# Optimization experiments

Hardware: AMD Instinct MI355X
Metric: run time of the kernel (lower is better)

The kernel has to match this reference:

```python
import jax, jax.numpy as jnp
import numpy as np

B, S, DIM, H = 8, 1024, 1024, 16
HID = 512  # FeedForward default hidden_dim=512 (module passes only dim)
DH = DIM // H
EPS = 1e-5


def setup_inputs() -> dict:
    key = jax.random.key(0)
    ks = jax.random.split(key, 12)
    s = 1.0 / np.sqrt(DIM)
    return {
        "x": jax.random.normal(ks[0], (B, S, DIM), dtype=jnp.float32),
        "Wq": jax.random.normal(ks[1], (DIM, DIM), dtype=jnp.float32) * s,
        "Wk": jax.random.normal(ks[2], (DIM, DIM), dtype=jnp.float32) * s,
        "Wv": jax.random.normal(ks[3], (DIM, DIM), dtype=jnp.float32) * s,
        "Wo": jax.random.normal(ks[4], (DIM, DIM), dtype=jnp.float32) * s,
        "ln1_g": jnp.ones((DIM,), jnp.float32),
        "ln1_b": jnp.zeros((DIM,), jnp.float32),
        "W1": jax.random.normal(ks[5], (DIM, HID), dtype=jnp.float32) * s,
        "b1": jnp.zeros((HID,), jnp.float32),
        "W2": jax.random.normal(ks[6], (HID, DIM), dtype=jnp.float32) * (1.0 / np.sqrt(HID)),
        "b2": jnp.zeros((DIM,), jnp.float32),
        "ln2_g": jnp.ones((DIM,), jnp.float32),
        "ln2_b": jnp.zeros((DIM,), jnp.float32),
    }


def _layer_norm(x, g, b):
    mu = jnp.mean(x, axis=-1, keepdims=True)
    var = jnp.mean(jnp.square(x - mu), axis=-1, keepdims=True)
    return (x - mu) * jax.lax.rsqrt(var + EPS) * g + b


def reference(x, Wq, Wk, Wv, Wo, ln1_g, ln1_b, W1, b1, W2, b2, ln2_g, ln2_b):
    # Multi-head self-attention (dropout = identity at eval)
    def heads(t):  # [B,S,DIM] -> [B,H,S,DH]
        return t.reshape(B, S, H, DH).transpose(0, 2, 1, 3)

    q = heads(x @ Wq)
    k = heads(x @ Wk)
    v = heads(x @ Wv)
    scores = jnp.einsum("bhqd,bhkd->bhqk", q, k) / jnp.sqrt(jnp.float32(DH))
    attn = jax.nn.softmax(scores, axis=-1)
    ctx = jnp.einsum("bhqk,bhkd->bhqd", attn, v)
    ctx = ctx.transpose(0, 2, 1, 3).reshape(B, S, DIM)
    mha = ctx @ Wo

    h = _layer_norm(mha + x, ln1_g, ln1_b)
    ff = jax.nn.relu(h @ W1 + b1) @ W2 + b2
    out = _layer_norm(ff + h, ln2_g, ln2_b)
    return out
```

## Files before the change

### kernel.cpp

```cpp
#include <hip/hip_runtime.h>
#include <cstdint>
#include <cstddef>

#define DEV __device__ __forceinline__

typedef __bf16 bf16x8 __attribute__((ext_vector_type(8)));
typedef __bf16 bf16x4 __attribute__((ext_vector_type(4)));
typedef short  short4v __attribute__((ext_vector_type(4)));
typedef float  f32x4  __attribute__((ext_vector_type(4)));

static constexpr int Bb  = 8;
static constexpr int S   = 1024;
static constexpr int DIM = 1024;
static constexpr int H   = 16;
static constexpr int DH  = 64;
static constexpr int HID = 512;
static constexpr int M   = Bb * S;

DEV uint16_t f2bf(float f) {
  union { float f; uint32_t u; } v; v.f = f;
  uint32_t r = v.u + 0x7fffu + ((v.u >> 16) & 1u);
  return (uint16_t)(r >> 16);
}
DEV float bf2f(uint32_t u) {
  union { uint32_t u; float f; } v; v.u = u << 16;
  return v.f;
}

DEV void gl_lds16(const uint16_t* g, uint16_t* lds) {
  __builtin_amdgcn_global_load_lds(
      (const __attribute__((address_space(1))) void*)g,
      (__attribute__((address_space(3))) void*)lds, 16, 0, 0);
}

DEV bf16x8 ld8(const uint16_t* p) { return *reinterpret_cast<const bf16x8*>(p); }

#if __has_builtin(__builtin_amdgcn_mfma_f32_16x16x16bf16_1k)
DEV f32x4 mfma16(bf16x4 a, bf16x4 b, f32x4 c) {
  return __builtin_amdgcn_mfma_f32_16x16x16bf16_1k(
      __builtin_bit_cast(short4v, a), __builtin_bit_cast(short4v, b), c, 0, 0, 0);
}
#else
DEV f32x4 mfma16(bf16x4 a, bf16x4 b, f32x4 c) {
  asm volatile("v_mfma_f32_16x16x16_bf16 %0, %1, %2, %0" : "+v"(c) : "v"(a), "v"(b));
  return c;
}
#endif

DEV int swz(int row, int col) {
  return row * 64 + (((col >> 3) ^ (row & 7)) << 3) + (col & 7);
}

__global__ __launch_bounds__(256) void prep_all(const float* __restrict__ x,
                                                uint16_t* __restrict__ x16,
                                                const float* __restrict__ Wq,
                                                const float* __restrict__ Wk,
                                                const float* __restrict__ Wv,
                                                const float* __restrict__ Wo,
                                                const float* __restrict__ W1,
                                                const float* __restrict__ W2,
                                                uint16_t* __restrict__ wqkv_t,
                                                uint16_t* __restrict__ wo_t,
                                                uint16_t* __restrict__ w1_t,
                                                uint16_t* __restrict__ w2_t) {
  int bid = blockIdx.x;
  int tid = threadIdx.x;
  if (bid < 4096) {
    int i = (bid * 256 + tid) * 8;
    const float4* p = reinterpret_cast<const float4*>(x + i);
    float4 a = p[0], b = p[1];
    uint4 pk;
    pk.x = (uint32_t)f2bf(a.x) | ((uint32_t)f2bf(a.y) << 16);
    pk.y = (uint32_t)f2bf(a.z) | ((uint32_t)f2bf(a.w) << 16);
    pk.z = (uint32_t)f2bf(b.x) | ((uint32_t)f2bf(b.y) << 16);
    pk.w = (uint32_t)f2bf(b.z) | ((uint32_t)f2bf(b.w) << 16);
    *reinterpret_cast<uint4*>(x16 + i) = pk;
    return;
  }
  bid -= 4096;
  const float* src;
  uint16_t* dst;
  int R, C, bx, by;
  if (bid < 4096) {
    int which = bid >> 10, id = bid & 1023;
    if (which == 0)      { src = Wq; dst = wqkv_t; }
    else if (which == 1) { src = Wk; dst = wqkv_t + 1048576; }
    else if (which == 2) { src = Wv; dst = wqkv_t + 2097152; }
    else                 { src = Wo; dst = wo_t; }
    R = 1024; C = 1024; bx = id & 31; by = id >> 5;
  } else if (bid < 4608) {
    int id = bid - 4096;
    src = W1; dst = w1_t; R = 1024; C = 512; bx = id & 15; by = id >> 4;
  } else {
    int id = bid - 4608;
    src = W2; dst = w2_t; R = 512; C = 1024; bx = id & 31; by = id >> 5;
  }
  __shared__ float tile[32][33];
  int c0 = bx * 32, r0 = by * 32;
  int tx = tid & 31, ty = tid >> 5;
  #pragma unroll
  for (int i = 0; i < 4; i++)
    tile[ty + i * 8][tx] = src[(size_t)(r0 + ty + i * 8) * C + c0 + tx];
  __syncthreads();
  #pragma unroll
  for (int i = 0; i < 4; i++)
    dst[(size_t)(c0 + ty + i * 8) * R + r0 + tx] = f2bf(tile[tx][ty + i * 8]);
}

template <int BIAS, int RELU, int FUSEV>
__global__ __launch_bounds__(256) void gemm128p(const uint16_t* __restrict__ A,
                                                const uint16_t* __restrict__ Bt,
                                                const float* __restrict__ bias,
                                                uint16_t* __restrict__ Cout,
                                                uint16_t* __restrict__ vt,
                                                int N, int K) {
  __shared__ __align__(16) uint16_t As[2][128 * 64];
  __shared__ __align__(16) uint16_t Bs[2][128 * 64];
  const int tid = threadIdx.x;
  const int w = tid >> 6, l = tid & 63;
  const int hi = l >> 4, c = l & 15;
  int nwg = gridDim.x * gridDim.y;
  int lin = blockIdx.y * gridDim.x + blockIdx.x;
  if (!(nwg & 7)) lin = (lin & 7) * (nwg >> 3) + (lin >> 3);
  const int bx = lin % gridDim.x, by = lin / gridDim.x;
  const int m0 = by * 128, n0 = bx * 128;
  const int wr = (w >> 1) * 64, wc = (w & 1) * 64;
  const uint16_t* Ag = A + (size_t)m0 * K;
  const uint16_t* Bg = Bt + (size_t)n0 * K;
  f32x4 acc[4][4] = {};

  const int srow = tid >> 3;
  const int scol = ((tid & 7) ^ (srow & 7)) * 8;
  auto stage = [&](int k0, int buf) {
    #pragma unroll
    for (int i = 0; i < 4; i++)
      gl_lds16(Ag + (size_t)(i * 32 + srow) * K + k0 + scol,
               &As[buf][(i * 256 + w * 64) * 8]);
    #pragma unroll
    for (int i = 0; i < 4; i++)
      gl_lds16(Bg + (size_t)(i * 32 + srow) * K + k0 + scol,
               &Bs[buf][(i * 256 + w * 64) * 8]);
  };

  stage(0, 0);
  stage(64, 1);
  asm volatile("s_waitcnt vmcnt(8)" ::: "memory");
  __builtin_amdgcn_s_barrier();

  const int NTK = K >> 6;
  for (int t = 0; t < NTK; t++) {
    const int cur = t & 1;
    const uint16_t* Ab = As[cur];
    const uint16_t* Bb = Bs[cur];
    bf16x8 af[4][2], bfr[4][2];
    #pragma unroll
    for (int i = 0; i < 4; i++)
      #pragma unroll
      for (int kk = 0; kk < 2; kk++) {
        af[i][kk]  = ld8(&Ab[swz(wr + i * 16 + c, kk * 32 + hi * 8)]);
        bfr[i][kk] = ld8(&Bb[swz(wc + i * 16 + c, kk * 32 + hi * 8)]);
      }
    #pragma unroll
    for (int i = 0; i < 4; i++)
      #pragma unroll
      for (int j = 0; j < 4; j++) {
        acc[i][j] = __builtin_amdgcn_mfma_f32_16x16x32_bf16(af[i][0], bfr[j][0], acc[i][j], 0, 0, 0);
        acc[i][j] = __builtin_amdgcn_mfma_f32_16x16x32_bf16(af[i][1], bfr[j][1], acc[i][j], 0, 0, 0);
      }
    if (t == NTK - 1) break;
    asm volatile("s_waitcnt lgkmcnt(0)" ::: "memory");
    __builtin_amdgcn_s_barrier();
    if (t + 2 < NTK) {
      stage((t + 2) << 6, cur);
      asm volatile("s_waitcnt vmcnt(8)" ::: "memory");
    } else {
      asm volatile("s_waitcnt vmcnt(0)" ::: "memory");
    }
    __builtin_amdgcn_s_barrier();
  }

  const int r0 = m0 + wr + hi * 4;
  const int c0 = n0 + wc + c;
  if (FUSEV && c0 >= 2048) {
    #pragma unroll
    for (int j = 0; j < 4; j++) {
      int hd = c0 + j * 16 - 2048;
      #pragma unroll
      for (int i = 0; i < 4; i++) {
        int row = r0 + i * 16;
        size_t vi = ((size_t)(row >> 10) * 1024 + hd) * 1024 + (row & 1023);
        uint2 pk;
        pk.x = (uint32_t)f2bf(acc[i][j][0]) | ((uint32_t)f2bf(acc[i][j][1]) << 16);
        pk.y = (uint32_t)f2bf(acc[i][j][2]) | ((uint32_t)f2bf(acc[i][j][3]) << 16);
        *(uint2*)&vt[vi] = pk;
      }
    }
  } else {
    #pragma unroll
    for (int j = 0; j < 4; j++) {
      int col = c0 + j * 16;
      float bv = BIAS ? bias[col] : 0.0f;
      #pragma unroll
      for (int i = 0; i < 4; i++) {
        #pragma unroll
        for (int r = 0; r < 4; r++) {
          float v = acc[i][j][r] + bv;
          if (RELU) v = fmaxf(v, 0.0f);
          Cout[(size_t)(r0 + i * 16 + r) * N + col] = f2bf(v);
        }
      }
    }
  }
}

__global__ __launch_bounds__(256, 4) void attn12(const uint16_t* __restrict__ qkv,
                                                 const uint16_t* __restrict__ vt,
                                                 uint16_t* __restrict__ ctx) {
  int blk = blockIdx.x;
  int xcd = blk & 7, idx = blk >> 3;
  int qt = idx & 7;
  int bh = xcd + 8 * (idx >> 3);
  int h = bh & 15, b = bh >> 4;
  int q0 = qt * 128;
  int tid = threadIdx.x;
  int w = tid >> 6, l = tid & 63;
  int hi = l >> 4, c = l & 15;

  __shared__ __align__(16) uint16_t Klds[2][64 * 64];
  __shared__ __align__(16) uint16_t Vlds[2][64 * 64];

  constexpr float C2 = 0.125f * 1.44269504f;
  const uint16_t* qbase = qkv + (size_t)(b * S + q0 + w * 32) * 3072 + h * 64;
  bf16x8 aq[2][2];
  #pragma unroll
  for (int qg = 0; qg < 2; qg++)
    #pragma unroll
    for (int dk = 0; dk < 2; dk++) {
      bf16x8 v = ld8(qbase + (size_t)(qg * 16 + c) * 3072 + dk * 32 + hi * 8);
      #pragma unroll
      for (int e = 0; e < 8; e++) v[e] = (__bf16)((float)v[e] * C2);
      aq[qg][dk] = v;
    }

  f32x4 acc[2][4] = {};
  float psum[2] = {};

  const uint16_t* kgbase = qkv + (size_t)(b * S) * 3072 + 1024 + h * 64;
  const uint16_t* vgbase = vt + (size_t)(b * 16 + h) * 64 * S;

  const int lr = l >> 3, lc = l & 7;
  const int scol = (lc ^ lr) * 8;
  auto stage = [&](int kt, int buf) {
    #pragma unroll
    for (int i = 0; i < 2; i++) {
      int slab = w * 2 + i;
      gl_lds16(kgbase + (size_t)(kt + slab * 8 + lr) * 3072 + scol,
               &Klds[buf][slab * 512]);
      gl_lds16(vgbase + (size_t)(slab * 8 + lr) * S + kt + scol,
               &Vlds[buf][slab * 512]);
    }
  };

  stage(0, 0);
  asm volatile("s_waitcnt vmcnt(0)" ::: "memory");
  __syncthreads();

  constexpr int NT = S / 64;
  for (int t = 0; t < NT; t++) {
    int cur = t & 1;
    if (t + 1 < NT) stage((t + 1) * 64, cur ^ 1);

    #pragma unroll
    for (int kb = 0; kb < 4; kb++) {
      bf16x8 kf0 = ld8(&Klds[cur][swz(kb * 16 + c, hi * 8)]);
      bf16x8 kf1 = ld8(&Klds[cur][swz(kb * 16 + c, 32 + hi * 8)]);
      bf16x4 pb[2];
      __builtin_amdgcn_s_setprio(1);
      f32x4 z0 = {0.f, 0.f, 0.f, 0.f}, z1 = {0.f, 0.f, 0.f, 0.f};
      z0 = __builtin_amdgcn_mfma_f32_16x16x32_bf16(kf0, aq[0][0], z0, 0, 0, 0);
      z0 = __builtin_amdgcn_mfma_f32_16x16x32_bf16(kf1, aq[0][1], z0, 0, 0, 0);
      z1 = __builtin_amdgcn_mfma_f32_16x16x32_bf16(kf0, aq[1][0], z1, 0, 0, 0);
      z1 = __builtin_amdgcn_mfma_f32_16x16x32_bf16(kf1, aq[1][1], z1, 0, 0, 0);
      __builtin_amdgcn_s_setprio(0);
      #pragma unroll
      for (int r = 0; r < 4; r++) {
        float p0 = exp2f(z0[r]);
        float p1 = exp2f(z1[r]);
        psum[0] += p0;
        psum[1] += p1;
        pb[0][r] = (__bf16)p0;
        pb[1][r] = (__bf16)p1;
      }
      __builtin_amdgcn_s_setprio(1);
      #pragma unroll
      for (int db = 0; db < 4; db++) {
        bf16x4 va = *(const bf16x4*)&Vlds[cur][swz(db * 16 + c, kb * 16 + hi * 4)];
        acc[0][db] = mfma16(va, pb[0], acc[0][db]);
        acc[1][db] = mfma16(va, pb[1], acc[1][db]);
      }
      __builtin_amdgcn_s_setprio(0);
    }

    if (t + 1 < NT) {
      asm volatile("s_waitcnt vmcnt(0)" ::: "memory");
      __syncthreads();
    }
  }

  #pragma unroll
  for (int qg = 0; qg < 2; qg++) {
    psum[qg] += __shfl_xor(psum[qg], 16);
    psum[qg] += __shfl_xor(psum[qg], 32);
  }

  __syncthreads();

  uint16_t* Bw = &Vlds[w >> 1][(w & 1) * 2048];
  #pragma unroll
  for (int qg = 0; qg < 2; qg++) {
    float inv = 1.0f / psum[qg];
    int q = qg * 16 + c;
    #pragma unroll
    for (int db = 0; db < 4; db++) {
      uint2 pk;
      pk.x = (uint32_t)f2bf(acc[qg][db][0] * inv) |
             ((uint32_t)f2bf(acc[qg][db][1] * inv) << 16);
      pk.y = (uint32_t)f2bf(acc[qg][db][2] * inv) |
             ((uint32_t)f2bf(acc[qg][db][3] * inv) << 16);
      int chunk4 = (db * 4 + hi) ^ (q & 15);
      *(uint2*)&Bw[q * 64 + chunk4 * 4] = pk;
    }
  }
  int rrow = l >> 3, rch = l & 7;
  size_t gq0 = (size_t)(b * S + q0 + w * 32);
  #pragma unroll
  for (int it = 0; it < 4; it++) {
    int row = it * 8 + rrow;
    int k0 = (2 * rch) ^ (row & 15);
    int base = (k0 & ~1) * 4;
    uint4 v = *(const uint4*)&Bw[row * 64 + base];
    if (row & 1) { uint32_t t0 = v.x, t1 = v.y; v.x = v.z; v.y = v.w; v.z = t0; v.w = t1; }
    *(uint4*)&ctx[(gq0 + row) * DIM + h * 64 + rch * 8] = v;
  }
}

__global__ __launch_bounds__(256) void ln1_w(const uint16_t* __restrict__ a16,
                                             const uint16_t* __restrict__ x16,
                                             const float* __restrict__ g,
                                             const float* __restrict__ beta,
                                             uint16_t* __restrict__ h16) {
  int w = threadIdx.x >> 6, l = threadIdx.x & 63;
  size_t row = (size_t)blockIdx.x * 4 + w;
  const uint16_t* ap = a16 + row * DIM + l * 16;
  const uint16_t* xp = x16 + row * DIM + l * 16;
  uint4 av0 = *(const uint4*)ap, av1 = *(const uint4*)(ap + 8);
  uint4 xv0 = *(const uint4*)xp, xv1 = *(const uint4*)(xp + 8);
  float v[16];
  const uint32_t* au0 = (const uint32_t*)&av0;
  const uint32_t* au1 = (const uint32_t*)&av1;
  const uint32_t* xu0 = (const uint32_t*)&xv0;
  const uint32_t* xu1 = (const uint32_t*)&xv1;
  #pragma unroll
  for (int j = 0; j < 4; j++) {
    v[j * 2]     = bf2f(au0[j] & 0xffff) + bf2f(xu0[j] & 0xffff);
    v[j * 2 + 1] = bf2f(au0[j] >> 16)    + bf2f(xu0[j] >> 16);
    v[8 + j * 2]     = bf2f(au1[j] & 0xffff) + bf2f(xu1[j] & 0xffff);
    v[8 + j * 2 + 1] = bf2f(au1[j] >> 16)    + bf2f(xu1[j] >> 16);
  }
  float s = 0.f, sq = 0.f;
  #pragma unroll
  for (int j = 0; j < 16; j++) { s += v[j]; sq += v[j] * v[j]; }
  #pragma unroll
  for (int off = 32; off >= 1; off >>= 1) {
    s += __shfl_xor(s, off);
    sq += __shfl_xor(sq, off);
  }
  float mu = s * (1.0f / DIM);
  float var = sq * (1.0f / DIM) - mu * mu;
  float rstd = rsqrtf(var + 1e-5f);
  const float4* gp = (const float4*)(g + l * 16);
  const float4* bp = (const float4*)(beta + l * 16);
  uint4 o0, o1;
  uint32_t* ou0 = (uint32_t*)&o0;
  uint32_t* ou1 = (uint32_t*)&o1;
  #pragma unroll
  for (int q = 0; q < 2; q++) {
    float4 gv = gp[q], bv = bp[q];
    float e0 = (v[q * 4 + 0] - mu) * rstd * gv.x + bv.x;
    float e1 = (v[q * 4 + 1] - mu) * rstd * gv.y + bv.y;
    float e2 = (v[q * 4 + 2] - mu) * rstd * gv.z + bv.z;
    float e3 = (v[q * 4 + 3] - mu) * rstd * gv.w + bv.w;
    ou0[q * 2]     = (uint32_t)f2bf(e0) | ((uint32_t)f2bf(e1) << 16);
    ou0[q * 2 + 1] = (uint32_t)f2bf(e2) | ((uint32_t)f2bf(e3) << 16);
    float4 gv2 = gp[2 + q], bv2 = bp[2 + q];
    float f0 = (v[8 + q * 4 + 0] - mu) * rstd * gv2.x + bv2.x;
    float f1 = (v[8 + q * 4 + 1] - mu) * rstd * gv2.y + bv2.y;
    float f2 = (v[8 + q * 4 + 2] - mu) * rstd * gv2.z + bv2.z;
    float f3 = (v[8 + q * 4 + 3] - mu) * rstd * gv2.w + bv2.w;
    ou1[q * 2]     = (uint32_t)f2bf(f0) | ((uint32_t)f2bf(f1) << 16);
    ou1[q * 2 + 1] = (uint32_t)f2bf(f2) | ((uint32_t)f2bf(f3) << 16);
  }
  uint16_t* hp = h16 + row * DIM + l * 16;
  *(uint4*)hp = o0;
  *(uint4*)(hp + 8) = o1;
}

__global__ __launch_bounds__(256) void ln2_w(const uint16_t* __restrict__ ff16,
                                             const uint16_t* __restrict__ h16,
                                             const float* __restrict__ g,
                                             const float* __restrict__ beta,
                                             float* __restrict__ out_f) {
  int w = threadIdx.x >> 6, l = threadIdx.x & 63;
  size_t row = (size_t)blockIdx.x * 4 + w;
  const uint16_t* ap = ff16 + row * DIM + l * 16;
  const uint16_t* xp = h16 + row * DIM + l * 16;
  uint4 av0 = *(const uint4*)ap, av1 = *(const uint4*)(ap + 8);
  uint4 xv0 = *(const uint4*)xp, xv1 = *(const uint4*)(xp + 8);
  float v[16];
  const uint32_t* au0 = (const uint32_t*)&av0;
  const uint32_t* au1 = (const uint32_t*)&av1;
  const uint32_t* xu0 = (const uint32_t*)&xv0;
  const uint32_t* xu1 = (const uint32_t*)&xv1;
  #pragma unroll
  for (int j = 0; j < 4; j++) {
    v[j * 2]     = bf2f(au0[j] & 0xffff) + bf2f(xu0[j] & 0xffff);
    v[j * 2 + 1] = bf2f(au0[j] >> 16)    + bf2f(xu0[j] >> 16);
    v[8 + j * 2]     = bf2f(au1[j] & 0xffff) + bf2f(xu1[j] & 0xffff);
    v[8 + j * 2 + 1] = bf2f(au1[j] >> 16)    + bf2f(xu1[j] >> 16);
  }
  float s = 0.f, sq = 0.f;
  #pragma unroll
  for (int j = 0; j < 16; j++) { s += v[j]; sq += v[j] * v[j]; }
  #pragma unroll
  for (int off = 32; off >= 1; off >>= 1) {
    s += __shfl_xor(s, off);
    sq += __shfl_xor(sq, off);
  }
  float mu = s * (1.0f / DIM);
  float var = sq * (1.0f / DIM) - mu * mu;
  float rstd = rsqrtf(var + 1e-5f);
  const float4* gp = (const float4*)(g + l * 16);
  const float4* bp = (const float4*)(beta + l * 16);
  float* op = out_f + row * DIM + l * 16;
  #pragma unroll
  for (int q = 0; q < 4; q++) {
    float4 gv = gp[q], bv = bp[q];
    float4 o;
    o.x = (v[q * 4 + 0] - mu) * rstd * gv.x + bv.x;
    o.y = (v[q * 4 + 1] - mu) * rstd * gv.y + bv.y;
    o.z = (v[q * 4 + 2] - mu) * rstd * gv.z + bv.z;
    o.w = (v[q * 4 + 3] - mu) * rstd * gv.w + bv.w;
    *(float4*)(op + q * 4) = o;
  }
}

extern "C" void kernel_launch(void* const* d_in, const int* in_sizes, int n_in,
                              void* d_out, int out_size, void* d_ws, size_t ws_size,
                              hipStream_t stream) {
  const float* x    = (const float*)d_in[0];
  const float* Wq   = (const float*)d_in[1];
  const float* Wk   = (const float*)d_in[2];
  const float* Wv   = (const float*)d_in[3];
  const float* Wo   = (const float*)d_in[4];
  const float* ln1g = (const float*)d_in[5];
  const float* ln1b = (const float*)d_in[6];
  const float* W1   = (const float*)d_in[7];
  const float* b1   = (const float*)d_in[8];
  const float* W2   = (const float*)d_in[9];
  const float* b2   = (const float*)d_in[10];
  const float* ln2g = (const float*)d_in[11];
  const float* ln2b = (const float*)d_in[12];
  float* out = (float*)d_out;

  char* ws = (char*)d_ws;
  uint16_t* wqkv_t = (uint16_t*)(ws + 0);
  uint16_t* wo_t   = (uint16_t*)(ws + 6291456);
  uint16_t* w1_t   = (uint16_t*)(ws + 8388608);
  uint16_t* w2_t   = (uint16_t*)(ws + 9437184);
  uint16_t* x16    = (uint16_t*)(ws + 10485760);
  uint16_t* qkv16  = (uint16_t*)(ws + 27262976);
  uint16_t* mha16  = (uint16_t*)(ws + 27262976);
  uint16_t* ff16   = (uint16_t*)(ws + 27262976);
  uint16_t* h16    = (uint16_t*)(ws + 60817408);
  uint16_t* vt16   = (uint16_t*)(ws + 77594624);
  uint16_t* mid16  = vt16;
  uint16_t* ctx16  = (uint16_t*)(ws + 94371840);

  prep_all<<<9216, 256, 0, stream>>>(x, x16, Wq, Wk, Wv, Wo, W1, W2,
                                     wqkv_t, wo_t, w1_t, w2_t);
  gemm128p<0, 0, 1><<<dim3(24, 64), 256, 0, stream>>>(x16, wqkv_t, nullptr,
                                                      qkv16, vt16, 3072, DIM);
  attn12<<<1024, 256, 0, stream>>>(qkv16, vt16, ctx16);
  gemm128p<0, 0, 0><<<dim3(8, 64), 256, 0, stream>>>(ctx16, wo_t, nullptr,
                                                     mha16, nullptr, DIM, DIM);
  ln1_w<<<2048, 256, 0, stream>>>(mha16, x16, ln1g, ln1b, h16);
  gemm128p<1, 1, 0><<<dim3(4, 64), 256, 0, stream>>>(h16, w1_t, b1,
                                                     mid16, nullptr, HID, DIM);
  gemm128p<1, 0, 0><<<dim3(8, 64), 256, 0, stream>>>(mid16, w2_t, b2,
                                                     ff16, nullptr, DIM, HID);
  ln2_w<<<2048, 256, 0, stream>>>(ff16, h16, ln2g, ln2b, out);
}
```

Before: 221.5 us.

## Use 256x256-tile 8-wave GEMM with interleaved staging for QKV projection

Adds a new GEMM kernel for the fused QKV projection. It uses 512 threads and 256x256 output tiles, with each wave computing 128x64. Global-to-LDS staging of the next A/B halves is interleaved between four MFMA phases, and s_setprio raises priority around the MFMA sections. The larger tile raises arithmetic intensity and cuts redundant global loads, at the cost of more LDS (128KB), more registers and fewer workgroups (384). The fused V-transpose epilogue moves into the new kernel and is dropped from the older template.

```diff
diff --git a/kernel.cpp b/kernel.cpp
--- a/kernel.cpp
+++ b/kernel.cpp
@@ -107,12 +107,175 @@
     dst[(size_t)(c0 + ty + i * 8) * R + r0 + tx] = f2bf(tile[tx][ty + i * 8]);
 }
 
-template <int BIAS, int RELU, int FUSEV>
+__global__ __launch_bounds__(512, 2) void gemm8p(const uint16_t* __restrict__ A,
+                                                 const uint16_t* __restrict__ Bt,
+                                                 uint16_t* __restrict__ Cout,
+                                                 uint16_t* __restrict__ vt,
+                                                 int N, int K) {
+  __shared__ __align__(16) uint16_t As[2][2][128 * 64];
+  __shared__ __align__(16) uint16_t Bs[2][2][128 * 64];
+  const int tid = threadIdx.x;
+  const int w = tid >> 6, l = tid & 63;
+  const int hi = l >> 4, c = l & 15;
+  const int wr = w >> 2, wc = w & 3;
+  int nwg = gridDim.x * gridDim.y;
+  int lin = blockIdx.y * gridDim.x + blockIdx.x;
+  if (!(nwg & 7)) lin = (lin & 7) * (nwg >> 3) + (lin >> 3);
+  const int bx = lin % gridDim.x, by = lin / gridDim.x;
+  const int m0 = by * 256, n0 = bx * 256;
+  const uint16_t* Ag = A + (size_t)m0 * K;
+  const uint16_t* Bg = Bt + (size_t)n0 * K;
+  f32x4 acc[8][4] = {};
+
+  const int srow = tid >> 3, sch = tid & 7;
+  auto stageA = [&](int kt, int d, int h) {
+    #pragma unroll
+    for (int i = 0; i < 2; i++) {
+      int slot = i * 512 + tid;
+      int row = slot >> 3, ch = slot & 7;
+      int scol = (ch ^ (row & 7)) * 8;
+      gl_lds16(Ag + (size_t)(h * 128 + row) * K + kt + scol, &As[d][h][slot * 8]);
+    }
+  };
+  auto stageB = [&](int kt, int d, int h) {
+    #pragma unroll
+    for (int i = 0; i < 2; i++) {
+      int slot = i * 512 + tid;
+      int row = slot >> 3, ch = slot & 7;
+      int scol = (ch ^ (row & 7)) * 8;
+      gl_lds16(Bg + (size_t)(h * 128 + row) * K + kt + scol, &Bs[d][h][slot * 8]);
+    }
+  };
+
+  stageA(0, 0, 0); stageA(0, 0, 1);
+  stageB(0, 0, 0); stageB(0, 0, 1);
+  stageB(64, 1, 0); stageB(64, 1, 1);
+  asm volatile("s_waitcnt vmcnt(4)" ::: "memory");
+  __builtin_amdgcn_s_barrier();
+
+  const int NT = K >> 6;
+  const int brow = (wc & 1) * 64;
+  bf16x8 af[4][2], bfr[4][2];
+  for (int t = 0; t < NT; t++) {
+    const int d = t & 1;
+    const uint16_t* Ah = As[d][wr];
+    const uint16_t* Bh = Bs[d][wc >> 1];
+
+    #pragma unroll
+    for (int mi = 0; mi < 4; mi++)
+      #pragma unroll
+      for (int kk = 0; kk < 2; kk++)
+        af[mi][kk] = ld8(&Ah[swz(mi * 16 + c, kk * 32 + hi * 8)]);
+    #pragma unroll
+    for (int ni = 0; ni < 2; ni++)
+      #pragma unroll
+      for (int kk = 0; kk < 2; kk++)
+        bfr[ni][kk] = ld8(&Bh[swz(brow + ni * 16 + c, kk * 32 + hi * 8)]);
+    if (t + 1 < NT) stageA((t + 1) << 6, d ^ 1, 0);
+    __builtin_amdgcn_s_barrier();
+    asm volatile("s_waitcnt lgkmcnt(0)" ::: "memory");
+    __builtin_amdgcn_s_setprio(1);
+    #pragma unroll
+    for (int mi = 0; mi < 4; mi++)
+      #pragma unroll
+      for (int ni = 0; ni < 2; ni++) {
+        acc[mi][ni] = __builtin_amdgcn_mfma_f32_16x16x32_bf16(af[mi][0], bfr[ni][0], acc[mi][ni], 0, 0, 0);
+        acc[mi][ni] = __builtin_amdgcn_mfma_f32_16x16x32_bf16(af[mi][1], bfr[ni][1], acc[mi][ni], 0, 0, 0);
+      }
+    __builtin_amdgcn_s_setprio(0);
+    __builtin_amdgcn_s_barrier();
+
+    #pragma unroll
+    for (int ni = 2; ni < 4; ni++)
+      #pragma unroll
+      for (int kk = 0; kk < 2; kk++)
+        bfr[ni][kk] = ld8(&Bh[swz(brow + ni * 16 + c, kk * 32 + hi * 8)]);
+    if (t + 1 < NT) stageA((t + 1) << 6, d ^ 1, 1);
+    __builtin_amdgcn_s_barrier();
+    asm volatile("s_waitcnt lgkmcnt(0)" ::: "memory");
+    __builtin_amdgcn_s_setprio(1);
+    #pragma unroll
+    for (int mi = 0; mi < 4; mi++)
+      #pragma unroll
+      for (int ni = 2; ni < 4; ni++) {
+        acc[mi][ni] = __builtin_amdgcn_mfma_f32_16x16x32_bf16(af[mi][0], bfr[ni][0], acc[mi][ni], 0, 0, 0);
+        acc[mi][ni] = __builtin_amdgcn_mfma_f32_16x16x32_bf16(af[mi][1], bfr[ni][1], acc[mi][ni], 0, 0, 0);
+      }
+    __builtin_amdgcn_s_setprio(0);
+    __builtin_amdgcn_s_barrier();
+
+    #pragma unroll
+    for (int mi = 0; mi < 4; mi++)
+      #pragma unroll
+      for (int kk = 0; kk < 2; kk++)
+        af[mi][kk] = ld8(&Ah[swz((mi + 4) * 16 + c, kk * 32 + hi * 8)]);
+    if (t + 2 < NT) stageB((t + 2) << 6, d, 0);
+    __builtin_amdgcn_s_barrier();
+    asm volatile("s_waitcnt lgkmcnt(0)" ::: "memory");
+    __builtin_amdgcn_s_setprio(1);
+    #pragma unroll
+    for (int mi = 0; mi < 4; mi++)
+      #pragma unroll
+      for (int ni = 0; ni < 2; ni++) {
+        acc[mi + 4][ni] = __builtin_amdgcn_mfma_f32_16x16x32_bf16(af[mi][0], bfr[ni][0], acc[mi + 4][ni], 0, 0, 0);
+        acc[mi + 4][ni] = __builtin_amdgcn_mfma_f32_16x16x32_bf16(af[mi][1], bfr[ni][1], acc[mi + 4][ni], 0, 0, 0);
+      }
+    __builtin_amdgcn_s_setprio(0);
+    __builtin_amdgcn_s_barrier();
+
+    if (t + 2 < NT) stageB((t + 2) << 6, d, 1);
+    __builtin_amdgcn_s_barrier();
+    __builtin_amdgcn_s_setprio(1);
+    #pragma unroll
+    for (int mi = 0; mi < 4; mi++)
+      #pragma unroll
+      for (int ni = 2; ni < 4; ni++) {
+        acc[mi + 4][ni] = __builtin_amdgcn_mfma_f32_16x16x32_bf16(af[mi][0], bfr[ni][0], acc[mi + 4][ni], 0, 0, 0);
+        acc[mi + 4][ni] = __builtin_amdgcn_mfma_f32_16x16x32_bf16(af[mi][1], bfr[ni][1], acc[mi + 4][ni], 0, 0, 0);
+      }
+    __builtin_amdgcn_s_setprio(0);
+    if (t + 1 < NT) {
+      if (t + 2 < NT) {
+        asm volatile("s_waitcnt vmcnt(4)" ::: "memory");
+      } else {
+        asm volatile("s_waitcnt vmcnt(0)" ::: "memory");
+      }
+      __builtin_amdgcn_s_barrier();
+    }
+  }
+
+  const int r0 = m0 + wr * 128 + hi * 4;
+  const int c0 = n0 + wc * 64 + c;
+  if (c0 >= 2048) {
+    #pragma unroll
+    for (int ni = 0; ni < 4; ni++) {
+      int hd = c0 + ni * 16 - 2048;
+      #pragma unroll
+      for (int mi = 0; mi < 8; mi++) {
+        int row = r0 + mi * 16;
+        size_t vi = ((size_t)(row >> 10) * 1024 + hd) * 1024 + (row & 1023);
+        uint2 pk;
+        pk.x = (uint32_t)f2bf(acc[mi][ni][0]) | ((uint32_t)f2bf(acc[mi][ni][1]) << 16);
+        pk.y = (uint32_t)f2bf(acc[mi][ni][2]) | ((uint32_t)f2bf(acc[mi][ni][3]) << 16);
+        *(uint2*)&vt[vi] = pk;
+      }
+    }
+  } else {
+    #pragma unroll
+    for (int mi = 0; mi < 8; mi++)
+      #pragma unroll
+      for (int ni = 0; ni < 4; ni++)
+        #pragma unroll
+        for (int r = 0; r < 4; r++)
+          Cout[(size_t)(r0 + mi * 16 + r) * N + c0 + ni * 16] = f2bf(acc[mi][ni][r]);
+  }
+}
+
+template <int BIAS, int RELU>
 __global__ __launch_bounds__(256) void gemm128p(const uint16_t* __restrict__ A,
                                                 const uint16_t* __restrict__ Bt,
                                                 const float* __restrict__ bias,
                                                 uint16_t* __restrict__ Cout,
-                                                uint16_t* __restrict__ vt,
                                                 int N, int K) {
   __shared__ __align__(16) uint16_t As[2][128 * 64];
   __shared__ __align__(16) uint16_t Bs[2][128 * 64];
@@ -181,33 +344,17 @@
 
   const int r0 = m0 + wr + hi * 4;
   const int c0 = n0 + wc + c;
-  if (FUSEV && c0 >= 2048) {
-    #pragma unroll
-    for (int j = 0; j < 4; j++) {
-      int hd = c0 + j * 16 - 2048;
-      #pragma unroll
-      for (int i = 0; i < 4; i++) {
-        int row = r0 + i * 16;
-        size_t vi = ((size_t)(row >> 10) * 1024 + hd) * 1024 + (row & 1023);
-        uint2 pk;
-        pk.x = (uint32_t)f2bf(acc[i][j][0]) | ((uint32_t)f2bf(acc[i][j][1]) << 16);
-        pk.y = (uint32_t)f2bf(acc[i][j][2]) | ((uint32_t)f2bf(acc[i][j][3]) << 16);
-        *(uint2*)&vt[vi] = pk;
-      }
-    }
-  } else {
-    #pragma unroll
-    for (int j = 0; j < 4; j++) {
-      int col = c0 + j * 16;
-      float bv = BIAS ? bias[col] : 0.0f;
-      #pragma unroll
-      for (int i = 0; i < 4; i++) {
-        #pragma unroll
-        for (int r = 0; r < 4; r++) {
-          float v = acc[i][j][r] + bv;
-          if (RELU) v = fmaxf(v, 0.0f);
-          Cout[(size_t)(r0 + i * 16 + r) * N + col] = f2bf(v);
-        }
+  #pragma unroll
+  for (int j = 0; j < 4; j++) {
+    int col = c0 + j * 16;
+    float bv = BIAS ? bias[col] : 0.0f;
+    #pragma unroll
+    for (int i = 0; i < 4; i++) {
+      #pragma unroll
+      for (int r = 0; r < 4; r++) {
+        float v = acc[i][j][r] + bv;
+        if (RELU) v = fmaxf(v, 0.0f);
+        Cout[(size_t)(r0 + i * 16 + r) * N + col] = f2bf(v);
       }
     }
   }
@@ -488,15 +635,14 @@
 
   prep_all<<<9216, 256, 0, stream>>>(x, x16, Wq, Wk, Wv, Wo, W1, W2,
                                      wqkv_t, wo_t, w1_t, w2_t);
-  gemm128p<0, 0, 1><<<dim3(24, 64), 256, 0, stream>>>(x16, wqkv_t, nullptr,
-                                                      qkv16, vt16, 3072, DIM);
+  gemm8p<<<dim3(12, 32), 512, 0, stream>>>(x16, wqkv_t, qkv16, vt16, 3072, DIM);
   attn12<<<1024, 256, 0, stream>>>(qkv16, vt16, ctx16);
-  gemm128p<0, 0, 0><<<dim3(8, 64), 256, 0, stream>>>(ctx16, wo_t, nullptr,
-                                                     mha16, nullptr, DIM, DIM);
+  gemm128p<0, 0><<<dim3(8, 64), 256, 0, stream>>>(ctx16, wo_t, nullptr,
+                                                  mha16, DIM, DIM);
   ln1_w<<<2048, 256, 0, stream>>>(mha16, x16, ln1g, ln1b, h16);
-  gemm128p<1, 1, 0><<<dim3(4, 64), 256, 0, stream>>>(h16, w1_t, b1,
-                                                     mid16, nullptr, HID, DIM);
-  gemm128p<1, 0, 0><<<dim3(8, 64), 256, 0, stream>>>(mid16, w2_t, b2,
-                                                     ff16, nullptr, DIM, HID);
+  gemm128p<1, 1><<<dim3(4, 64), 256, 0, stream>>>(h16, w1_t, b1,
+                                                  mid16, HID, DIM);
+  gemm128p<1, 0><<<dim3(8, 64), 256, 0, stream>>>(mid16, w2_t, b2,
+                                                  ff16, DIM, HID);
   ln2_w<<<2048, 256, 0, stream>>>(ff16, h16, ln2g, ln2b, out);
 }
```

Measured after the change: 230.1 us. 3.9% more time.
